# Performance work log

Hardware: AMD Instinct MI355X
Metric: run time of the kernel (lower is better)

The kernel has to match this reference:

```python
import jax, jax.numpy as jnp
import numpy as np


def setup_inputs() -> dict:
    key = jax.random.key(0)
    k1, k2 = jax.random.split(key)
    STATE_LEN, SEQ_LEN, HIDDEN = 8192, 8192, 1024
    out_state = jax.random.normal(k1, (STATE_LEN, HIDDEN), dtype=jnp.float32)
    history = jax.random.normal(k2, (SEQ_LEN, HIDDEN), dtype=jnp.float32)
    return {"out_state": out_state, "history": history}


def reference(out_state, history):
    # attn_energies[i, j] = dot(out_state[i], history[j])  ->  single GEMM
    energies = jnp.einsum('ih,jh->ij', out_state, history)  # [state_len, seq_len]
    # legacy F.softmax on a 2D tensor normalizes along dim=1 (the seq_len axis)
    return jax.nn.softmax(energies, axis=-1)
```

## Files before the change

### kernel.cpp

```cpp
#include <hip/hip_runtime.h>
#include <hip/hip_bf16.h>

#define M 8192
#define N 8192
#define K 1024
#define BM 256
#define BN 256
#define BK 32
#define KT (K/BK)

typedef __attribute__((ext_vector_type(8))) short short8;
typedef __attribute__((ext_vector_type(4))) float f32x4;
typedef __attribute__((ext_vector_type(16))) float f32x16;

__device__ inline short f2bf(float x){
    __hip_bfloat16 h = __float2bfloat16(x);
    short s; __builtin_memcpy(&s, &h, 2); return s;
}
__device__ inline float bf2f(short s){
    __hip_bfloat16 h; __builtin_memcpy(&h, &s, 2);
    return __bfloat162float(h);
}

__device__ inline void conv8(float4 x0, float4 x1, short8& hi, short8& lo){
    float xs[8] = {x0.x,x0.y,x0.z,x0.w,x1.x,x1.y,x1.z,x1.w};
    #pragma unroll
    for (int j=0;j<8;++j){
        short h = f2bf(xs[j]);
        float r = xs[j] - bf2f(h);
        hi[j] = h; lo[j] = f2bf(r);
    }
}

#define GLOAD_LDS16(gp, lp) \
    __builtin_amdgcn_global_load_lds((const __attribute__((address_space(1))) void*)(gp), \
                                     (__attribute__((address_space(3))) void*)(lp), 16, 0, 0)

__global__ __launch_bounds__(512) void presplit_t(
    const float* __restrict__ A, const float* __restrict__ B,
    short* __restrict__ Aht, short* __restrict__ Alt,
    short* __restrict__ Bht, short* __restrict__ Blt)
{
    size_t c = (size_t)blockIdx.x * 512 + threadIdx.x;
    const float* src; short *dh, *dl;
    const size_t perMat = (size_t)M * (K/8);
    if (c < perMat){ src = A; dh = Aht; dl = Alt; }
    else { c -= perMat; src = B; dh = Bht; dl = Blt; }
    int row = (int)(c >> 7);
    int k8  = (int)(c & 127);
    const float* p = src + (size_t)row * K + k8 * 8;
    float4 x0 = *(const float4*)p;
    float4 x1 = *(const float4*)(p + 4);
    short8 hi, lo; conv8(x0, x1, hi, lo);
    size_t o = ((size_t)k8 * M + row) * 8;
    *(short8*)(dh + o) = hi;
    *(short8*)(dl + o) = lo;
}

__global__ __launch_bounds__(512, 2)
void gemm_t(const short* __restrict__ Aht, const short* __restrict__ Alt,
            const short* __restrict__ Bht, const short* __restrict__ Blt,
            float* __restrict__ C)
{
    __shared__ __align__(16) short lds[2][4][4][BM][8];

    const int tid  = threadIdx.x;
    const int lane = tid & 63, wid = tid >> 6;

    const int xcd = blockIdx.x & 7;
    const int gid = xcd * 128 + (blockIdx.x >> 3);
    const int bm0 = (gid >> 5) * BM;
    const int bn0 = (gid & 31) * BN;

    const int wr = wid >> 2, wc = wid & 3;
    const int fr = lane & 31;
    const int fg = lane >> 5;

    const int arr = wid >> 1;
    const short* gp = (arr == 0) ? Aht : (arr == 1) ? Alt : (arr == 2) ? Bht : Blt;
    const int   gb  = (arr < 2) ? bm0 : bn0;
    const int sbase = (wid & 1) * 2;

    f32x16 acc[4][2] = {};

    auto STAGE = [&](int buf, int kt){
        #pragma unroll
        for (int i = 0; i < 8; ++i){
            int s  = sbase + (i >> 2);
            int rb = i & 3;
            const short* src = gp + (((size_t)(kt * 4 + s)) * M + gb + rb * 64 + lane) * 8;
            GLOAD_LDS16(src, &lds[buf][arr][s][rb * 64][0]);
        }
    };

    STAGE(0, 0);
    __syncthreads();
    int cur = 0;

    for (int kt = 0; kt < KT; ++kt){
        if (kt + 1 < KT) STAGE(cur ^ 1, kt + 1);

        short8 bh0[2], bl0[2], ah0[4], al0[4];
        #pragma unroll
        for (int n = 0; n < 2; ++n){
            int row = wc * 64 + n * 32 + fr;
            bh0[n] = *(const short8*)&lds[cur][2][fg][row][0];
            bl0[n] = *(const short8*)&lds[cur][3][fg][row][0];
        }
        #pragma unroll
        for (int m = 0; m < 4; ++m){
            int row = wr * 128 + m * 32 + fr;
            ah0[m] = *(const short8*)&lds[cur][0][fg][row][0];
            al0[m] = *(const short8*)&lds[cur][1][fg][row][0];
        }

        short8 bh1[2], bl1[2], ah1[4], al1[4];
        #pragma unroll
        for (int n = 0; n < 2; ++n){
            int row = wc * 64 + n * 32 + fr;
            bh1[n] = *(const short8*)&lds[cur][2][2 + fg][row][0];
            bl1[n] = *(const short8*)&lds[cur][3][2 + fg][row][0];
        }
        #pragma unroll
        for (int m = 0; m < 4; ++m){
            int row = wr * 128 + m * 32 + fr;
            ah1[m] = *(const short8*)&lds[cur][0][2 + fg][row][0];
            al1[m] = *(const short8*)&lds[cur][1][2 + fg][row][0];
        }

        __builtin_amdgcn_s_setprio(1);
        #pragma unroll
        for (int m = 0; m < 4; ++m){
            #pragma unroll
            for (int n = 0; n < 2; ++n){
                acc[m][n] = __builtin_amdgcn_mfma_f32_32x32x16_bf16(ah0[m], bh0[n], acc[m][n], 0, 0, 0);
                acc[m][n] = __builtin_amdgcn_mfma_f32_32x32x16_bf16(ah0[m], bl0[n], acc[m][n], 0, 0, 0);
                acc[m][n] = __builtin_amdgcn_mfma_f32_32x32x16_bf16(al0[m], bh0[n], acc[m][n], 0, 0, 0);
            }
        }
        #pragma unroll
        for (int m = 0; m < 4; ++m){
            #pragma unroll
            for (int n = 0; n < 2; ++n){
                acc[m][n] = __builtin_amdgcn_mfma_f32_32x32x16_bf16(ah1[m], bh1[n], acc[m][n], 0, 0, 0);
                acc[m][n] = __builtin_amdgcn_mfma_f32_32x32x16_bf16(ah1[m], bl1[n], acc[m][n], 0, 0, 0);
                acc[m][n] = __builtin_amdgcn_mfma_f32_32x32x16_bf16(al1[m], bh1[n], acc[m][n], 0, 0, 0);
            }
        }
        __builtin_amdgcn_s_setprio(0);

        __syncthreads();
        cur ^= 1;
    }

    #pragma unroll
    for (int m = 0; m < 4; ++m){
        #pragma unroll
        for (int n = 0; n < 2; ++n){
            #pragma unroll
            for (int g = 0; g < 4; ++g){
                #pragma unroll
                for (int r = 0; r < 4; ++r){
                    int row = r + 8 * g + 4 * fg;
                    C[(size_t)(bm0 + wr * 128 + m * 32 + row) * N
                      + bn0 + wc * 64 + n * 32 + fr] = acc[m][n][g * 4 + r];
                }
            }
        }
    }
}

#define FBM 128
#define FBN 128
#define FBK 64
#define FARR (FBM*FBK)
__global__ __launch_bounds__(256, 2)
void gemm_fb(const float* __restrict__ A, const float* __restrict__ B,
             float* __restrict__ C)
{
    __shared__ __align__(16) short sAh[FARR];
    __shared__ __align__(16) short sAl[FARR];
    __shared__ __align__(16) short sBh[FARR];
    __shared__ __align__(16) short sBl[FARR];

    const int tid  = threadIdx.x;
    const int lane = tid & 63, wid = tid >> 6;
    const int bm0 = blockIdx.y * FBM, bn0 = blockIdx.x * FBN;
    const int wr = wid >> 1, wc = wid & 1;
    const int fr = lane & 15, fg = lane >> 4;

    f32x4 acc[4][4] = {};

    for (int kt = 0; kt < K/FBK; ++kt){
        #pragma unroll
        for (int i = 0; i < 4; ++i){
            int s = tid + i * 256;
            int row = s >> 3, sp = s & 7;
            int widx = row * FBK + ((sp ^ (row & 7)) << 3);
            const float* ga = A + (size_t)(bm0 + row) * K + kt * FBK + sp * 8;
            float4 a0 = *(const float4*)ga, a1 = *(const float4*)(ga + 4);
            short8 hi, lo;
            conv8(a0, a1, hi, lo);
            *(short8*)&sAh[widx] = hi;
            *(short8*)&sAl[widx] = lo;
            const float* gbp = B + (size_t)(bn0 + row) * K + kt * FBK + sp * 8;
            float4 b0 = *(const float4*)gbp, b1 = *(const float4*)(gbp + 4);
            conv8(b0, b1, hi, lo);
            *(short8*)&sBh[widx] = hi;
            *(short8*)&sBl[widx] = lo;
        }
        __syncthreads();

        #pragma unroll
        for (int ks = 0; ks < 2; ++ks){
            short8 ah[4], al[4], bh[4], bl[4];
            #pragma unroll
            for (int m = 0; m < 4; ++m){
                int row = wr * 64 + m * 16 + fr;
                int idx = row * FBK + ((((ks << 2) | fg) ^ (row & 7)) << 3);
                ah[m] = *(const short8*)&sAh[idx];
                al[m] = *(const short8*)&sAl[idx];
            }
            #pragma unroll
            for (int n = 0; n < 4; ++n){
                int row = wc * 64 + n * 16 + fr;
                int idx = row * FBK + ((((ks << 2) | fg) ^ (row & 7)) << 3);
                bh[n] = *(const short8*)&sBh[idx];
                bl[n] = *(const short8*)&sBl[idx];
            }
            #pragma unroll
            for (int m = 0; m < 4; ++m){
                #pragma unroll
                for (int n = 0; n < 4; ++n){
                    acc[m][n] = __builtin_amdgcn_mfma_f32_16x16x32_bf16(ah[m], bh[n], acc[m][n], 0, 0, 0);
                    acc[m][n] = __builtin_amdgcn_mfma_f32_16x16x32_bf16(ah[m], bl[n], acc[m][n], 0, 0, 0);
                    acc[m][n] = __builtin_amdgcn_mfma_f32_16x16x32_bf16(al[m], bh[n], acc[m][n], 0, 0, 0);
                }
            }
        }
        __syncthreads();
    }

    #pragma unroll
    for (int m = 0; m < 4; ++m){
        int grow = bm0 + wr * 64 + m * 16 + fg * 4;
        #pragma unroll
        for (int r = 0; r < 4; ++r){
            float* crow = C + (size_t)(grow + r) * N + bn0 + wc * 64 + fr;
            #pragma unroll
            for (int n = 0; n < 4; ++n)
                crow[n * 16] = acc[m][n][r];
        }
    }
}

__global__ __launch_bounds__(256) void softmax_fused(float* __restrict__ E)
{
    const int row = blockIdx.x;
    const int tid = threadIdx.x;
    const int lane = tid & 63, wid = tid >> 6;
    float4* rp = (float4*)(E + (size_t)row * N);
    float4 v[8];
    float mx = -3.4e38f;
    #pragma unroll
    for (int i = 0; i < 8; ++i){
        v[i] = rp[tid + i * 256];
        mx = fmaxf(mx, fmaxf(fmaxf(v[i].x, v[i].y), fmaxf(v[i].z, v[i].w)));
    }
    #pragma unroll
    for (int off = 32; off; off >>= 1) mx = fmaxf(mx, __shfl_xor(mx, off));
    __shared__ float redm[4], reds[4];
    if (lane == 0) redm[wid] = mx;
    __syncthreads();
    mx = fmaxf(fmaxf(redm[0], redm[1]), fmaxf(redm[2], redm[3]));
    float s = 0.f;
    #pragma unroll
    for (int i = 0; i < 8; ++i){
        v[i].x = __expf(v[i].x - mx); v[i].y = __expf(v[i].y - mx);
        v[i].z = __expf(v[i].z - mx); v[i].w = __expf(v[i].w - mx);
        s += v[i].x + v[i].y + v[i].z + v[i].w;
    }
    #pragma unroll
    for (int off = 32; off; off >>= 1) s += __shfl_xor(s, off);
    if (lane == 0) reds[wid] = s;
    __syncthreads();
    float inv = 1.0f / (reds[0] + reds[1] + reds[2] + reds[3]);
    #pragma unroll
    for (int i = 0; i < 8; ++i){
        float4 o = v[i];
        o.x *= inv; o.y *= inv; o.z *= inv; o.w *= inv;
        rp[tid + i * 256] = o;
    }
}

extern "C" void kernel_launch(void* const* d_in, const int* in_sizes, int n_in,
                              void* d_out, int out_size, void* d_ws, size_t ws_size,
                              hipStream_t stream)
{
    const float* A = (const float*)d_in[0];
    const float* B = (const float*)d_in[1];
    float* out = (float*)d_out;

    const size_t elems = (size_t)M * K;
    const size_t splitBytes = 4 * elems * sizeof(short);

    if (ws_size >= splitBytes){
        short* Aht = (short*)d_ws;
        short* Alt = Aht + elems;
        short* Bht = Alt + elems;
        short* Blt = Bht + elems;
        presplit_t<<<4096, 512, 0, stream>>>(A, B, Aht, Alt, Bht, Blt);
        gemm_t<<<(M/BM)*(N/BN), 512, 0, stream>>>(Aht, Alt, Bht, Blt, out);
    } else {
        gemm_fb<<<dim3(N/FBN, M/FBM), 256, 0, stream>>>(A, B, out);
    }
    softmax_fused<<<M, 256, 0, stream>>>(out);
}
```

Before: 487.6 us.

## Shrink GEMM tile to 256x128 with single-buffered LDS and grouped block swizzle

Cuts the GEMM block tile from 256x256 to 256x128 and the block from 512 to 256 threads (4 waves). Drops the LDS double buffer in favour of a single buffer with a sync after each load. Changes the block-to-tile mapping so each XCD works on 4x4 groups of neighbouring tiles. The smaller LDS footprint is meant to raise occupancy and improve L2 locality, but removing the double buffer exposes global-load latency in every k-step.

```diff
diff --git a/kernel.cpp b/kernel.cpp
--- a/kernel.cpp
+++ b/kernel.cpp
@@ -5,7 +5,7 @@
 #define N 8192
 #define K 1024
 #define BM 256
-#define BN 256
+#define BN 128
 #define BK 32
 #define KT (K/BK)
 
@@ -57,100 +57,82 @@
     *(short8*)(dl + o) = lo;
 }
 
-__global__ __launch_bounds__(512, 2)
+__global__ __launch_bounds__(256, 2)
 void gemm_t(const short* __restrict__ Aht, const short* __restrict__ Alt,
             const short* __restrict__ Bht, const short* __restrict__ Blt,
             float* __restrict__ C)
 {
-    __shared__ __align__(16) short lds[2][4][4][BM][8];
+    __shared__ __align__(16) short sAh[4][BM][8];
+    __shared__ __align__(16) short sAl[4][BM][8];
+    __shared__ __align__(16) short sBh[4][BN][8];
+    __shared__ __align__(16) short sBl[4][BN][8];
 
     const int tid  = threadIdx.x;
     const int lane = tid & 63, wid = tid >> 6;
 
     const int xcd = blockIdx.x & 7;
-    const int gid = xcd * 128 + (blockIdx.x >> 3);
-    const int bm0 = (gid >> 5) * BM;
-    const int bn0 = (gid & 31) * BN;
-
-    const int wr = wid >> 2, wc = wid & 3;
+    const int idx = blockIdx.x >> 3;
+    const int stg = xcd * 16 + (idx >> 4);
+    const int pos = idx & 15;
+    const int bm0 = ((stg >> 4) * 4 + (pos >> 2)) * BM;
+    const int bn0 = ((stg & 15) * 4 + (pos & 3)) * BN;
+
+    const int wr = wid >> 1, wc = wid & 1;
     const int fr = lane & 31;
     const int fg = lane >> 5;
 
-    const int arr = wid >> 1;
-    const short* gp = (arr == 0) ? Aht : (arr == 1) ? Alt : (arr == 2) ? Bht : Blt;
-    const int   gb  = (arr < 2) ? bm0 : bn0;
-    const int sbase = (wid & 1) * 2;
-
     f32x16 acc[4][2] = {};
 
-    auto STAGE = [&](int buf, int kt){
-        #pragma unroll
-        for (int i = 0; i < 8; ++i){
-            int s  = sbase + (i >> 2);
-            int rb = i & 3;
-            const short* src = gp + (((size_t)(kt * 4 + s)) * M + gb + rb * 64 + lane) * 8;
-            GLOAD_LDS16(src, &lds[buf][arr][s][rb * 64][0]);
+    auto STAGE = [&](int kt){
+        #pragma unroll
+        for (int i = 0; i < 4; ++i){
+            int gl = i * 256 + tid;
+            size_t g = ((size_t)(kt * 4 + (gl >> 8))) * M + bm0 + (gl & 255);
+            GLOAD_LDS16(Aht + g * 8, &sAh[0][0][0] + gl * 8);
+            GLOAD_LDS16(Alt + g * 8, &sAl[0][0][0] + gl * 8);
+        }
+        #pragma unroll
+        for (int i = 0; i < 2; ++i){
+            int gl = i * 256 + tid;
+            size_t g = ((size_t)(kt * 4 + (gl >> 7))) * M + bn0 + (gl & 127);
+            GLOAD_LDS16(Bht + g * 8, &sBh[0][0][0] + gl * 8);
+            GLOAD_LDS16(Blt + g * 8, &sBl[0][0][0] + gl * 8);
         }
     };
 
-    STAGE(0, 0);
-    __syncthreads();
-    int cur = 0;
-
     for (int kt = 0; kt < KT; ++kt){
-        if (kt + 1 < KT) STAGE(cur ^ 1, kt + 1);
-
-        short8 bh0[2], bl0[2], ah0[4], al0[4];
-        #pragma unroll
-        for (int n = 0; n < 2; ++n){
-            int row = wc * 64 + n * 32 + fr;
-            bh0[n] = *(const short8*)&lds[cur][2][fg][row][0];
-            bl0[n] = *(const short8*)&lds[cur][3][fg][row][0];
-        }
-        #pragma unroll
-        for (int m = 0; m < 4; ++m){
-            int row = wr * 128 + m * 32 + fr;
-            ah0[m] = *(const short8*)&lds[cur][0][fg][row][0];
-            al0[m] = *(const short8*)&lds[cur][1][fg][row][0];
-        }
-
-        short8 bh1[2], bl1[2], ah1[4], al1[4];
-        #pragma unroll
-        for (int n = 0; n < 2; ++n){
-            int row = wc * 64 + n * 32 + fr;
-            bh1[n] = *(const short8*)&lds[cur][2][2 + fg][row][0];
-            bl1[n] = *(const short8*)&lds[cur][3][2 + fg][row][0];
-        }
-        #pragma unroll
-        for (int m = 0; m < 4; ++m){
-            int row = wr * 128 + m * 32 + fr;
-            ah1[m] = *(const short8*)&lds[cur][0][2 + fg][row][0];
-            al1[m] = *(const short8*)&lds[cur][1][2 + fg][row][0];
-        }
-
-        __builtin_amdgcn_s_setprio(1);
-        #pragma unroll
-        for (int m = 0; m < 4; ++m){
+        STAGE(kt);
+        __syncthreads();
+
+        #pragma unroll
+        for (int ks = 0; ks < 2; ++ks){
+            const int slot = 2 * ks + fg;
+            short8 ah[4], al[4], bh[2], bl[2];
             #pragma unroll
             for (int n = 0; n < 2; ++n){
-                acc[m][n] = __builtin_amdgcn_mfma_f32_32x32x16_bf16(ah0[m], bh0[n], acc[m][n], 0, 0, 0);
-                acc[m][n] = __builtin_amdgcn_mfma_f32_32x32x16_bf16(ah0[m], bl0[n], acc[m][n], 0, 0, 0);
-                acc[m][n] = __builtin_amdgcn_mfma_f32_32x32x16_bf16(al0[m], bh0[n], acc[m][n], 0, 0, 0);
-            }
-        }
-        #pragma unroll
-        for (int m = 0; m < 4; ++m){
-            #pragma unroll
-            for (int n = 0; n < 2; ++n){
-                acc[m][n] = __builtin_amdgcn_mfma_f32_32x32x16_bf16(ah1[m], bh1[n], acc[m][n], 0, 0, 0);
-                acc[m][n] = __builtin_amdgcn_mfma_f32_32x32x16_bf16(ah1[m], bl1[n], acc[m][n], 0, 0, 0);
-                acc[m][n] = __builtin_amdgcn_mfma_f32_32x32x16_bf16(al1[m], bh1[n], acc[m][n], 0, 0, 0);
-            }
-        }
-        __builtin_amdgcn_s_setprio(0);
-
+                int row = wc * 64 + n * 32 + fr;
+                bh[n] = *(const short8*)&sBh[slot][row][0];
+                bl[n] = *(const short8*)&sBl[slot][row][0];
+            }
+            #pragma unroll
+            for (int m = 0; m < 4; ++m){
+                int row = wr * 128 + m * 32 + fr;
+                ah[m] = *(const short8*)&sAh[slot][row][0];
+                al[m] = *(const short8*)&sAl[slot][row][0];
+            }
+            __builtin_amdgcn_s_setprio(1);
+            #pragma unroll
+            for (int m = 0; m < 4; ++m){
+                #pragma unroll
+                for (int n = 0; n < 2; ++n){
+                    acc[m][n] = __builtin_amdgcn_mfma_f32_32x32x16_bf16(ah[m], bh[n], acc[m][n], 0, 0, 0);
+                    acc[m][n] = __builtin_amdgcn_mfma_f32_32x32x16_bf16(ah[m], bl[n], acc[m][n], 0, 0, 0);
+                    acc[m][n] = __builtin_amdgcn_mfma_f32_32x32x16_bf16(al[m], bh[n], acc[m][n], 0, 0, 0);
+                }
+            }
+            __builtin_amdgcn_s_setprio(0);
+        }
         __syncthreads();
-        cur ^= 1;
     }
 
     #pragma unroll
@@ -310,7 +292,7 @@
         short* Bht = Alt + elems;
         short* Blt = Bht + elems;
         presplit_t<<<4096, 512, 0, stream>>>(A, B, Aht, Alt, Bht, Blt);
-        gemm_t<<<(M/BM)*(N/BN), 512, 0, stream>>>(Aht, Alt, Bht, Blt, out);
+        gemm_t<<<(M/BM)*(N/BN), 256, 0, stream>>>(Aht, Alt, Bht, Blt, out);
     } else {
         gemm_fb<<<dim3(N/FBN, M/FBM), 256, 0, stream>>>(A, B, out);
     }
```

Result: faster. 470.1 us (-3.6%).
